# Performance work log

Hardware: AMD Instinct MI355X
Metric: run time of the kernel (lower is better)

## Reference

```python
import jax, jax.numpy as jnp
import numpy as np

BETA = 1.0 / np.sqrt(768.0).astype(np.float32)


def setup_inputs() -> dict:
    key = jax.random.key(0)
    k1, k2, k3 = jax.random.split(key, 3)
    x = jax.random.normal(k1, (32, 512, 768), dtype=jnp.float32)
    # torch nn.Linear(dim, n_prototype).weight has shape [n_prototype, dim]
    w_lookup = jax.random.normal(k2, (4096, 768), dtype=jnp.float32) * 0.02
    # torch nn.Linear(n_prototype, dim).weight has shape [dim, n_prototype]
    w_content = jax.random.normal(k3, (768, 4096), dtype=jnp.float32) * 0.02
    return {"x": x, "w_lookup": w_lookup, "w_content": w_content}


def reference(x, w_lookup, w_content):
    # scores: [b, s, n_prototype] = x @ w_lookup^T, scaled by 1/sqrt(dim)
    scores = jnp.einsum("bsd,pd->bsp", x, w_lookup) * jnp.asarray(BETA, x.dtype)
    lookup = jax.nn.softmax(scores, axis=-1)
    # content: [b, s, dim] = lookup @ w_content^T
    content = jnp.einsum("bsp,dp->bsd", lookup, w_content)
    return content  # dropout is identity in eval / p=0.0
```

## Files before the change

kernel.cpp:

```cpp
#include <hip/hip_runtime.h>
#include <hip/hip_bf16.h>


#define NTOK   16384
#define DIM    768
#define NPROT  4096
#define BETA_F 0.03608439182428583f

typedef __bf16 bf16_t;
typedef __bf16 bf16x8 __attribute__((ext_vector_type(8)));
typedef float  floatx4 __attribute__((ext_vector_type(4)));

__device__ __forceinline__ void async_copy16(const bf16_t* g, void* l) {
  __builtin_amdgcn_global_load_lds(
      (__attribute__((address_space(1))) const void*)g,
      (__attribute__((address_space(3))) void*)l, 16, 0, 0);
}

__global__ __launch_bounds__(256) void cvt_all(
    const float* __restrict__ x, const float* __restrict__ wl,
    const float* __restrict__ wc, bf16_t* __restrict__ xb,
    bf16_t* __restrict__ wlb, bf16_t* __restrict__ wcb,
    int nx8, int nw8, int nc8) {
  int i = blockIdx.x * 256 + threadIdx.x;
  const float* in; bf16_t* out; int k; int dv;
  if (i < nx8) {
    in = x; out = xb; k = i;
    const int m = k / 96, kv = k % 96;
    const int kt = kv >> 3, kr = kv & 7;
    const int sf = (((m >> 4) & 15) << 1) + (kr >> 2);
    const int l  = (m & 15) + ((kr & 3) << 4);
    dv = (((m >> 8) * 12 + kt) * 32 + sf) * 64 + l;
  } else if (i < nx8 + nw8) {
    in = wl; out = wlb; k = i - nx8;
    const int p = k / 96, kv = k % 96;
    const int kt = kv >> 3, kr = kv & 7;
    const int sf = (((p >> 4) & 15) << 1) + (kr >> 2);
    const int l  = (p & 15) + ((kr & 3) << 4);
    dv = (((p >> 8) * 12 + kt) * 32 + sf) * 64 + l;
  } else if (i < nx8 + nw8 + nc8) {
    in = wc; out = wcb; k = i - nx8 - nw8;
    const int d = k / 512, pv = k % 512;
    const int kt = pv >> 3, kr = pv & 7;
    const int dd = d % 192;
    const int sf = ((dd >> 4) << 1) + (kr >> 2);
    const int l  = (dd & 15) + ((kr & 3) << 4);
    dv = (((d / 192) * 64 + kt) * 24 + sf) * 64 + l;
  } else return;
  const float4* in4 = (const float4*)in;
  float4 a = in4[2 * k], b = in4[2 * k + 1];
  bf16x8 o;
  o[0] = (bf16_t)a.x; o[1] = (bf16_t)a.y; o[2] = (bf16_t)a.z; o[3] = (bf16_t)a.w;
  o[4] = (bf16_t)b.x; o[5] = (bf16_t)b.y; o[6] = (bf16_t)b.z; o[7] = (bf16_t)b.w;
  ((bf16x8*)out)[dv] = o;
}

__global__ __launch_bounds__(512, 2)
void gemm256(const bf16_t* __restrict__ A, const bf16_t* __restrict__ B,
             bf16_t* __restrict__ P, float* __restrict__ rowsum,
             const int K, const int N, const int nN) {
  __shared__ char lds[131072];

  const int tid = threadIdx.x;
  const int l   = tid & 63;
  const int w   = tid >> 6;
  const int wr  = w >> 2;
  const int wc  = w & 3;
  const int lr  = l & 15;

  const int nwg   = gridDim.x;
  const int chunk = nwg >> 3;
  const int wg    = (blockIdx.x & 7) * chunk + (blockIdx.x >> 3);
  const int m0    = (wg / nN) * 256;
  const int n0    = (wg % nN) * 256;

  const int T = K >> 6;
  const int abase = (m0 >> 8) * T * 16384 + l * 8;
  const int bbase = (n0 >> 8) * T * 16384 + l * 8;
  int asf[2][2];
#pragma unroll
  for (int h = 0; h < 2; ++h)
#pragma unroll
    for (int j = 0; j < 2; ++j) {
      const int s = j * 8 + w;
      asf[h][j] = ((h * 8 + (s >> 1)) * 2 + (s & 1)) * 512;
    }

  auto stageA = [&](int slot, int kt, int h) {
#pragma unroll
    for (int j = 0; j < 2; ++j) {
      const int s  = j * 8 + w;
      const int sf = (h * 8 + (s >> 1)) * 2 + (s & 1);
      async_copy16(A + abase + kt * 16384 + asf[h][j],
                   lds + slot * 65536 + sf * 1024);
    }
  };
  auto stageB = [&](int slot, int kt, int h) {
#pragma unroll
    for (int j = 0; j < 2; ++j) {
      const int s  = j * 8 + w;
      const int sf = (h * 8 + (s >> 1)) * 2 + (s & 1);
      async_copy16(B + bbase + kt * 16384 + asf[h][j],
                   lds + slot * 65536 + 32768 + sf * 1024);
    }
  };

  bf16x8 af[4][2], bg[4][2];
  auto loadA = [&](int slot, int mh) {
#pragma unroll
    for (int q = 0; q < 4; ++q)
#pragma unroll
      for (int ks = 0; ks < 2; ++ks)
        af[q][ks] = *(const bf16x8*)(lds + slot * 65536 +
                        ((mh * 8 + q * 2 + wr) * 2 + ks) * 1024 + l * 16);
  };
  auto loadB = [&](int slot, int nh, int qb) {
#pragma unroll
    for (int q = 0; q < 2; ++q)
#pragma unroll
      for (int ks = 0; ks < 2; ++ks)
        bg[qb + q][ks] = *(const bf16x8*)(lds + slot * 65536 + 32768 +
                        ((nh * 8 + q * 4 + wc) * 2 + ks) * 1024 + l * 16);
  };

  const floatx4 z = {0.f, 0.f, 0.f, 0.f};
  floatx4 acc[8][4];
#pragma unroll
  for (int mt = 0; mt < 8; ++mt)
#pragma unroll
    for (int nt = 0; nt < 4; ++nt) acc[mt][nt] = z;

  auto mma = [&](int mq, int nq) {
    __builtin_amdgcn_s_setprio(1);
#pragma unroll
    for (int q = 0; q < 4; ++q)
#pragma unroll
      for (int r = 0; r < 2; ++r)
#pragma unroll
        for (int ks = 0; ks < 2; ++ks)
          acc[mq * 4 + q][nq * 2 + r] = __builtin_amdgcn_mfma_f32_16x16x32_bf16(
              af[q][ks], bg[nq * 2 + r][ks], acc[mq * 4 + q][nq * 2 + r], 0, 0, 0);
    __builtin_amdgcn_s_setprio(0);
  };

#define BAR()    __builtin_amdgcn_s_barrier()
#define LGKM0()  asm volatile("s_waitcnt lgkmcnt(0)")
#define LGKM8()  asm volatile("s_waitcnt lgkmcnt(8)")
#define VM(n)    asm volatile("s_waitcnt vmcnt(" #n ")" ::: "memory")

  stageA(0, 0, 0); stageB(0, 0, 0); stageB(0, 0, 1); stageA(0, 0, 1);
  stageA(1, 1, 0); stageB(1, 1, 0); stageB(1, 1, 1);
  VM(6);
  BAR();

#pragma unroll 1
  for (int t = 0; t < T - 2; t += 2) {
    loadA(0, 0); loadB(0, 0, 0);
    stageA(1, t + 1, 1);
    LGKM8();
    BAR(); LGKM0(); mma(0, 0); BAR();
    loadB(0, 1, 2);
    stageA(0, t + 2, 0);
    BAR(); LGKM0(); mma(0, 1); BAR();
    loadA(0, 1);
    stageB(0, t + 2, 0);
    BAR(); LGKM0(); mma(1, 1); BAR();
    stageB(0, t + 2, 1);
    BAR(); mma(1, 0); VM(6); BAR();
    loadA(1, 0); loadB(1, 0, 0);
    stageA(0, t + 2, 1);
    LGKM8();
    BAR(); LGKM0(); mma(0, 0); BAR();
    loadB(1, 1, 2);
    stageA(1, t + 3, 0);
    BAR(); LGKM0(); mma(0, 1); BAR();
    loadA(1, 1);
    stageB(1, t + 3, 0);
    BAR(); LGKM0(); mma(1, 1); BAR();
    stageB(1, t + 3, 1);
    BAR(); mma(1, 0); VM(6); BAR();
  }

  loadA(0, 0); loadB(0, 0, 0);
  stageA(1, T - 1, 1);
  LGKM8();
  BAR(); LGKM0(); mma(0, 0); BAR();
  loadB(0, 1, 2);
  BAR(); LGKM0(); mma(0, 1); BAR();
  loadA(0, 1);
  BAR(); LGKM0(); mma(1, 1); BAR();
  BAR(); mma(1, 0); VM(0); BAR();
  loadA(1, 0); loadB(1, 0, 0);
  BAR(); LGKM0(); mma(0, 0); BAR();
  loadB(1, 1, 2);
  BAR(); LGKM0(); mma(0, 1); BAR();
  loadA(1, 1);
  BAR(); LGKM0(); mma(1, 1); BAR();
  mma(1, 0);

#undef BAR
#undef LGKM0
#undef LGKM8
#undef VM

  __syncthreads();
  bf16_t* pl = (bf16_t*)lds;
  const int hi4 = (l >> 4) << 2;
#pragma unroll
  for (int mt = 0; mt < 8; ++mt) {
    const int rl = (mt * 2 + wr) * 16 + hi4;
    float rs[4] = {0.f, 0.f, 0.f, 0.f};
#pragma unroll
    for (int nt = 0; nt < 4; ++nt) {
      const int cl = (nt * 4 + wc) * 16 + lr;
#pragma unroll
      for (int i = 0; i < 4; ++i) {
        const float e = __expf(acc[mt][nt][i] * BETA_F);
        pl[(rl + i) * 256 + cl] = (bf16_t)e;
        rs[i] += e;
      }
    }
#pragma unroll
    for (int i = 0; i < 4; ++i) {
      float s = rs[i];
      s += __shfl_xor(s, 1);
      s += __shfl_xor(s, 2);
      s += __shfl_xor(s, 4);
      s += __shfl_xor(s, 8);
      if (lr == 0) atomicAdd(&rowsum[m0 + rl + i], s);
    }
  }
  __syncthreads();
#pragma unroll
  for (int it = 0; it < 16; ++it) {
    const int idx = it * 512 + tid;
    const int rr  = idx >> 5;
    const int cc  = (idx & 31) << 3;
    bf16x8 v = *(const bf16x8*)(pl + rr * 256 + cc);
    *(bf16x8*)(P + (size_t)(m0 + rr) * N + n0 + cc) = v;
  }
}

__global__ __launch_bounds__(512, 2)
void gemm192(const bf16_t* __restrict__ A, const bf16_t* __restrict__ B,
             float* __restrict__ O, const float* __restrict__ rowsum,
             const int K, const int N) {
  __shared__ char lds[114688];

  const int tid = threadIdx.x;
  const int l   = tid & 63;
  const int w   = tid >> 6;
  const int wr  = w >> 2;
  const int wc  = w & 3;
  const int lr  = l & 15;
  const int lk  = (l >> 4) << 3;

  const int wg = (blockIdx.x & 7) * 32 + (blockIdx.x >> 3);
  const int m0 = (wg >> 2) * 256;
  const int n0 = (wg & 3) * 192;

  int aoff[2][2];
#pragma unroll
  for (int h = 0; h < 2; ++h)
#pragma unroll
    for (int j = 0; j < 2; ++j) {
      const int s     = j * 8 + w;
      const int mfrag = h * 8 + (s >> 1);
      const int ks    = s & 1;
      aoff[h][j] = (m0 + mfrag * 16 + lr) * K + ks * 32 + lk;
    }
  const int bb = (n0 / 192) * 64 * 12288 + l * 8;
  int bsf[3];
#pragma unroll
  for (int t = 0; t < 3; ++t) bsf[t] = (t * 8 + w) * 512;

  auto stageA = [&](int slot, int kt, int h) {
#pragma unroll
    for (int j = 0; j < 2; ++j) {
      const int s  = j * 8 + w;
      const int sf = (h * 8 + (s >> 1)) * 2 + (s & 1);
      async_copy16(A + aoff[h][j] + kt * 64, lds + slot * 57344 + sf * 1024);
    }
  };
  auto stageBt = [&](int slot, int kt, int t) {
    async_copy16(B + bb + kt * 12288 + bsf[t],
                 lds + slot * 57344 + 32768 + (t * 8 + w) * 1024 + l * 16);
  };

  bf16x8 af[4][2], bg[3][2];
  auto loadA = [&](int slot, int mh) {
#pragma unroll
    for (int q = 0; q < 4; ++q)
#pragma unroll
      for (int ks = 0; ks < 2; ++ks)
        af[q][ks] = *(const bf16x8*)(lds + slot * 57344 +
                        ((mh * 8 + q * 2 + wr) * 2 + ks) * 1024 + l * 16);
  };
  auto loadBn = [&](int slot, int nlo, int ncnt) {
    for (int r = 0; r < ncnt; ++r)
#pragma unroll
      for (int ks = 0; ks < 2; ++ks)
        bg[nlo + r][ks] = *(const bf16x8*)(lds + slot * 57344 + 32768 +
                        (((wc * 3 + nlo + r) * 2 + ks) << 10) + l * 16);
  };

  const floatx4 z = {0.f, 0.f, 0.f, 0.f};
  floatx4 acc[8][3];
#pragma unroll
  for (int mt = 0; mt < 8; ++mt)
#pragma unroll
    for (int nt = 0; nt < 3; ++nt) acc[mt][nt] = z;

  auto mma = [&](int mq, int nlo, int ncnt) {
    __builtin_amdgcn_s_setprio(1);
#pragma unroll
    for (int q = 0; q < 4; ++q)
      for (int r = 0; r < ncnt; ++r)
#pragma unroll
        for (int ks = 0; ks < 2; ++ks)
          acc[mq * 4 + q][nlo + r] = __builtin_amdgcn_mfma_f32_16x16x32_bf16(
              af[q][ks], bg[nlo + r][ks], acc[mq * 4 + q][nlo + r], 0, 0, 0);
    __builtin_amdgcn_s_setprio(0);
  };

#define BAR()    __builtin_amdgcn_s_barrier()
#define LGKM0()  asm volatile("s_waitcnt lgkmcnt(0)")
#define LGKM8()  asm volatile("s_waitcnt lgkmcnt(8)")
#define VM(n)    asm volatile("s_waitcnt vmcnt(" #n ")" ::: "memory")

  const int T = K >> 6;

  stageA(0, 0, 0); stageA(0, 0, 1);
  stageBt(0, 0, 0); stageBt(0, 0, 1); stageBt(0, 0, 2);
  stageA(1, 1, 0);
  stageBt(1, 1, 0); stageBt(1, 1, 1); stageBt(1, 1, 2);
  VM(5);
  BAR();

#pragma unroll 1
  for (int t = 0; t < T - 2; t += 2) {
#pragma unroll
    for (int u = 0; u < 2; ++u) {
      const int p = u;
      loadA(p, 0); loadBn(p, 0, 2);
      stageA(p ^ 1, t + u + 1, 1);
      LGKM8();
      BAR(); LGKM0(); mma(0, 0, 2); BAR();
      loadBn(p, 2, 1);
      stageA(p, t + u + 2, 0);
      BAR(); LGKM0(); mma(0, 2, 1); BAR();
      loadA(p, 1);
      stageBt(p, t + u + 2, 0); stageBt(p, t + u + 2, 1);
      BAR(); LGKM0(); mma(1, 0, 2); BAR();
      stageBt(p, t + u + 2, 2);
      BAR(); mma(1, 2, 1); VM(5); BAR();
    }
  }

  loadA(0, 0); loadBn(0, 0, 2);
  stageA(1, T - 1, 1);
  LGKM8();
  BAR(); LGKM0(); mma(0, 0, 2); BAR();
  loadBn(0, 2, 1);
  BAR(); LGKM0(); mma(0, 2, 1); BAR();
  loadA(0, 1);
  BAR(); LGKM0(); mma(1, 0, 2); BAR();
  BAR(); mma(1, 2, 1); VM(0); BAR();
  loadA(1, 0); loadBn(1, 0, 2);
  BAR(); LGKM0(); mma(0, 0, 2); BAR();
  loadBn(1, 2, 1);
  BAR(); LGKM0(); mma(0, 2, 1); BAR();
  loadA(1, 1);
  BAR(); LGKM0(); mma(1, 0, 2); BAR();
  mma(1, 2, 1);

#undef BAR
#undef LGKM0
#undef LGKM8
#undef VM

  const int hi4 = (l >> 4) << 2;
#pragma unroll
  for (int mt = 0; mt < 8; ++mt) {
    const int row = m0 + (mt * 2 + wr) * 16 + hi4;
#pragma unroll
    for (int i = 0; i < 4; ++i) {
      const float inv = 1.0f / rowsum[row + i];
#pragma unroll
      for (int nt = 0; nt < 3; ++nt)
        O[(row + i) * N + n0 + (wc * 3 + nt) * 16 + lr] = acc[mt][nt][i] * inv;
    }
  }
}

__global__ __launch_bounds__(256) void hopfield_fallback(
    const float* __restrict__ x, const float* __restrict__ wl,
    const float* __restrict__ wc, float* __restrict__ out) {
  __shared__ float  xs[8 * 768];
  __shared__ bf16_t ps[8 * 4096];
  __shared__ float  rs[8];
  const int tid = threadIdx.x;
  const int r0  = blockIdx.x * 8;
  if (tid < 8) rs[tid] = 0.f;
  for (int i = tid; i < 8 * 768; i += 256)
    xs[i] = x[(r0 + (i / 768)) * 768 + (i % 768)];
  __syncthreads();

  float lsum[8] = {0, 0, 0, 0, 0, 0, 0, 0};
  for (int p = tid; p < 4096; p += 256) {
    float s[8] = {0, 0, 0, 0, 0, 0, 0, 0};
    for (int d = 0; d < 768; ++d) {
      const float wv = wl[p * 768 + d];
#pragma unroll
      for (int r = 0; r < 8; ++r) s[r] += xs[r * 768 + d] * wv;
    }
#pragma unroll
    for (int r = 0; r < 8; ++r) {
      const float e = __expf(s[r] * BETA_F);
      ps[r * 4096 + p] = (bf16_t)e;
      lsum[r] += e;
    }
  }
#pragma unroll
  for (int r = 0; r < 8; ++r) atomicAdd(&rs[r], lsum[r]);
  __syncthreads();

  for (int d = tid; d < 768; d += 256) {
    float o[8] = {0, 0, 0, 0, 0, 0, 0, 0};
    for (int p = 0; p < 4096; ++p) {
      const float wv = wc[d * 4096 + p];
#pragma unroll
      for (int r = 0; r < 8; ++r) o[r] += (float)ps[r * 4096 + p] * wv;
    }
#pragma unroll
    for (int r = 0; r < 8; ++r) out[(r0 + r) * 768 + d] = o[r] / rs[r];
  }
}

extern "C" void kernel_launch(void* const* d_in, const int* in_sizes, int n_in,
                              void* d_out, int out_size, void* d_ws, size_t ws_size,
                              hipStream_t stream) {
  (void)in_sizes; (void)n_in; (void)out_size;
  const float* x  = (const float*)d_in[0];
  const float* wl = (const float*)d_in[1];
  const float* wc = (const float*)d_in[2];
  float* out = (float*)d_out;

  const size_t xb_e = (size_t)NTOK * DIM;
  const size_t wl_e = (size_t)NPROT * DIM;
  const size_t wc_e = (size_t)DIM * NPROT;
  const size_t P_e  = (size_t)NTOK * NPROT;
  const size_t need = (xb_e + wl_e + wc_e + P_e) * 2 + (size_t)NTOK * 4;

  if (ws_size >= need) {
    char* ws = (char*)d_ws;
    bf16_t* xb  = (bf16_t*)ws;  ws += xb_e * 2;
    bf16_t* wlb = (bf16_t*)ws;  ws += wl_e * 2;
    bf16_t* wcb = (bf16_t*)ws;  ws += wc_e * 2;
    bf16_t* P   = (bf16_t*)ws;  ws += P_e * 2;
    float* rowsum = (float*)ws;

    hipMemsetAsync(rowsum, 0, NTOK * sizeof(float), stream);
    const int nx8 = (int)(xb_e / 8), nw8 = (int)(wl_e / 8), nc8 = (int)(wc_e / 8);
    cvt_all<<<(nx8 + nw8 + nc8 + 255) / 256, 256, 0, stream>>>(
        x, wl, wc, xb, wlb, wcb, nx8, nw8, nc8);
    gemm256<<<dim3((NTOK / 256) * (NPROT / 256)), 512, 0, stream>>>(
        xb, wlb, P, rowsum, DIM, NPROT, NPROT / 256);
    gemm192<<<dim3(256), 512, 0, stream>>>(
        P, wcb, out, rowsum, NPROT, DIM);
  } else {
    hopfield_fallback<<<NTOK / 8, 256, 0, stream>>>(x, wl, wc, out);
  }
}
```

Before: 388.2 us.

## Restructure GEMM main loops into two-phase schedule with full B fragment loads

```diff
diff --git a/kernel.cpp b/kernel.cpp
--- a/kernel.cpp
+++ b/kernel.cpp
@@ -114,13 +114,15 @@
         af[q][ks] = *(const bf16x8*)(lds + slot * 65536 +
                         ((mh * 8 + q * 2 + wr) * 2 + ks) * 1024 + l * 16);
   };
-  auto loadB = [&](int slot, int nh, int qb) {
-#pragma unroll
-    for (int q = 0; q < 2; ++q)
-#pragma unroll
-      for (int ks = 0; ks < 2; ++ks)
-        bg[qb + q][ks] = *(const bf16x8*)(lds + slot * 65536 + 32768 +
-                        ((nh * 8 + q * 4 + wc) * 2 + ks) * 1024 + l * 16);
+  auto loadB = [&](int slot) {
+#pragma unroll
+    for (int nh = 0; nh < 2; ++nh)
+#pragma unroll
+      for (int q = 0; q < 2; ++q)
+#pragma unroll
+        for (int ks = 0; ks < 2; ++ks)
+          bg[nh * 2 + q][ks] = *(const bf16x8*)(lds + slot * 65536 + 32768 +
+                          ((nh * 8 + q * 4 + wc) * 2 + ks) * 1024 + l * 16);
   };
 
   const floatx4 z = {0.f, 0.f, 0.f, 0.f};
@@ -130,77 +132,57 @@
 #pragma unroll
     for (int nt = 0; nt < 4; ++nt) acc[mt][nt] = z;
 
-  auto mma = [&](int mq, int nq) {
+  auto mma2 = [&](int mq) {
     __builtin_amdgcn_s_setprio(1);
 #pragma unroll
-    for (int q = 0; q < 4; ++q)
-#pragma unroll
-      for (int r = 0; r < 2; ++r)
-#pragma unroll
-        for (int ks = 0; ks < 2; ++ks)
-          acc[mq * 4 + q][nq * 2 + r] = __builtin_amdgcn_mfma_f32_16x16x32_bf16(
-              af[q][ks], bg[nq * 2 + r][ks], acc[mq * 4 + q][nq * 2 + r], 0, 0, 0);
+    for (int ks = 0; ks < 2; ++ks)
+#pragma unroll
+      for (int q = 0; q < 4; ++q)
+#pragma unroll
+        for (int nt = 0; nt < 4; ++nt)
+          acc[mq * 4 + q][nt] = __builtin_amdgcn_mfma_f32_16x16x32_bf16(
+              af[q][ks], bg[nt][ks], acc[mq * 4 + q][nt], 0, 0, 0);
     __builtin_amdgcn_s_setprio(0);
   };
 
 #define BAR()    __builtin_amdgcn_s_barrier()
 #define LGKM0()  asm volatile("s_waitcnt lgkmcnt(0)")
-#define LGKM8()  asm volatile("s_waitcnt lgkmcnt(8)")
 #define VM(n)    asm volatile("s_waitcnt vmcnt(" #n ")" ::: "memory")
 
-  stageA(0, 0, 0); stageB(0, 0, 0); stageB(0, 0, 1); stageA(0, 0, 1);
+  stageA(0, 0, 0); stageA(0, 0, 1); stageB(0, 0, 0); stageB(0, 0, 1);
   stageA(1, 1, 0); stageB(1, 1, 0); stageB(1, 1, 1);
   VM(6);
   BAR();
 
 #pragma unroll 1
-  for (int t = 0; t < T - 2; t += 2) {
-    loadA(0, 0); loadB(0, 0, 0);
-    stageA(1, t + 1, 1);
-    LGKM8();
-    BAR(); LGKM0(); mma(0, 0); BAR();
-    loadB(0, 1, 2);
-    stageA(0, t + 2, 0);
-    BAR(); LGKM0(); mma(0, 1); BAR();
-    loadA(0, 1);
-    stageB(0, t + 2, 0);
-    BAR(); LGKM0(); mma(1, 1); BAR();
-    stageB(0, t + 2, 1);
-    BAR(); mma(1, 0); VM(6); BAR();
-    loadA(1, 0); loadB(1, 0, 0);
-    stageA(0, t + 2, 1);
-    LGKM8();
-    BAR(); LGKM0(); mma(0, 0); BAR();
-    loadB(1, 1, 2);
-    stageA(1, t + 3, 0);
-    BAR(); LGKM0(); mma(0, 1); BAR();
-    loadA(1, 1);
-    stageB(1, t + 3, 0);
-    BAR(); LGKM0(); mma(1, 1); BAR();
-    stageB(1, t + 3, 1);
-    BAR(); mma(1, 0); VM(6); BAR();
-  }
-
-  loadA(0, 0); loadB(0, 0, 0);
-  stageA(1, T - 1, 1);
-  LGKM8();
-  BAR(); LGKM0(); mma(0, 0); BAR();
-  loadB(0, 1, 2);
-  BAR(); LGKM0(); mma(0, 1); BAR();
-  loadA(0, 1);
-  BAR(); LGKM0(); mma(1, 1); BAR();
-  BAR(); mma(1, 0); VM(0); BAR();
-  loadA(1, 0); loadB(1, 0, 0);
-  BAR(); LGKM0(); mma(0, 0); BAR();
-  loadB(1, 1, 2);
-  BAR(); LGKM0(); mma(0, 1); BAR();
-  loadA(1, 1);
-  BAR(); LGKM0(); mma(1, 1); BAR();
-  mma(1, 0);
+  for (int t = 0; t < T - 2; ++t) {
+    const int p = t & 1;
+    loadA(p, 0); loadB(p);
+    stageA(p ^ 1, t + 1, 1);
+    BAR(); LGKM0(); mma2(0); BAR();
+    loadA(p, 1);
+    stageA(p, t + 2, 0);
+    stageB(p, t + 2, 0); stageB(p, t + 2, 1);
+    BAR(); LGKM0(); mma2(1);
+    VM(6);
+    BAR();
+  }
+
+  {
+    const int p = (T - 2) & 1;
+    loadA(p, 0); loadB(p);
+    stageA(p ^ 1, T - 1, 1);
+    BAR(); LGKM0(); mma2(0); BAR();
+    loadA(p, 1);
+    BAR(); LGKM0(); mma2(1); VM(0); BAR();
+    loadA(p ^ 1, 0); loadB(p ^ 1);
+    BAR(); LGKM0(); mma2(0); BAR();
+    loadA(p ^ 1, 1);
+    BAR(); LGKM0(); mma2(1);
+  }
 
 #undef BAR
 #undef LGKM0
-#undef LGKM8
 #undef VM
 
   __syncthreads();
@@ -296,12 +278,13 @@
         af[q][ks] = *(const bf16x8*)(lds + slot * 57344 +
                         ((mh * 8 + q * 2 + wr) * 2 + ks) * 1024 + l * 16);
   };
-  auto loadBn = [&](int slot, int nlo, int ncnt) {
-    for (int r = 0; r < ncnt; ++r)
+  auto loadBall = [&](int slot) {
+#pragma unroll
+    for (int r = 0; r < 3; ++r)
 #pragma unroll
       for (int ks = 0; ks < 2; ++ks)
-        bg[nlo + r][ks] = *(const bf16x8*)(lds + slot * 57344 + 32768 +
-                        (((wc * 3 + nlo + r) * 2 + ks) << 10) + l * 16);
+        bg[r][ks] = *(const bf16x8*)(lds + slot * 57344 + 32768 +
+                        (((wc * 3 + r) * 2 + ks) << 10) + l * 16);
   };
 
   const floatx4 z = {0.f, 0.f, 0.f, 0.f};
@@ -311,21 +294,21 @@
 #pragma unroll
     for (int nt = 0; nt < 3; ++nt) acc[mt][nt] = z;
 
-  auto mma = [&](int mq, int nlo, int ncnt) {
+  auto mma2 = [&](int mq) {
     __builtin_amdgcn_s_setprio(1);
 #pragma unroll
-    for (int q = 0; q < 4; ++q)
-      for (int r = 0; r < ncnt; ++r)
-#pragma unroll
-        for (int ks = 0; ks < 2; ++ks)
-          acc[mq * 4 + q][nlo + r] = __builtin_amdgcn_mfma_f32_16x16x32_bf16(
-              af[q][ks], bg[nlo + r][ks], acc[mq * 4 + q][nlo + r], 0, 0, 0);
+    for (int ks = 0; ks < 2; ++ks)
+#pragma unroll
+      for (int q = 0; q < 4; ++q)
+#pragma unroll
+        for (int nt = 0; nt < 3; ++nt)
+          acc[mq * 4 + q][nt] = __builtin_amdgcn_mfma_f32_16x16x32_bf16(
+              af[q][ks], bg[nt][ks], acc[mq * 4 + q][nt], 0, 0, 0);
     __builtin_amdgcn_s_setprio(0);
   };
 
 #define BAR()    __builtin_amdgcn_s_barrier()
 #define LGKM0()  asm volatile("s_waitcnt lgkmcnt(0)")
-#define LGKM8()  asm volatile("s_waitcnt lgkmcnt(8)")
 #define VM(n)    asm volatile("s_waitcnt vmcnt(" #n ")" ::: "memory")
 
   const int T = K >> 6;
@@ -338,45 +321,34 @@
   BAR();
 
 #pragma unroll 1
-  for (int t = 0; t < T - 2; t += 2) {
-#pragma unroll
-    for (int u = 0; u < 2; ++u) {
-      const int p = u;
-      loadA(p, 0); loadBn(p, 0, 2);
-      stageA(p ^ 1, t + u + 1, 1);
-      LGKM8();
-      BAR(); LGKM0(); mma(0, 0, 2); BAR();
-      loadBn(p, 2, 1);
-      stageA(p, t + u + 2, 0);
-      BAR(); LGKM0(); mma(0, 2, 1); BAR();
-      loadA(p, 1);
-      stageBt(p, t + u + 2, 0); stageBt(p, t + u + 2, 1);
-      BAR(); LGKM0(); mma(1, 0, 2); BAR();
-      stageBt(p, t + u + 2, 2);
-      BAR(); mma(1, 2, 1); VM(5); BAR();
-    }
-  }
-
-  loadA(0, 0); loadBn(0, 0, 2);
-  stageA(1, T - 1, 1);
-  LGKM8();
-  BAR(); LGKM0(); mma(0, 0, 2); BAR();
-  loadBn(0, 2, 1);
-  BAR(); LGKM0(); mma(0, 2, 1); BAR();
-  loadA(0, 1);
-  BAR(); LGKM0(); mma(1, 0, 2); BAR();
-  BAR(); mma(1, 2, 1); VM(0); BAR();
-  loadA(1, 0); loadBn(1, 0, 2);
-  BAR(); LGKM0(); mma(0, 0, 2); BAR();
-  loadBn(1, 2, 1);
-  BAR(); LGKM0(); mma(0, 2, 1); BAR();
-  loadA(1, 1);
-  BAR(); LGKM0(); mma(1, 0, 2); BAR();
-  mma(1, 2, 1);
+  for (int t = 0; t < T - 2; ++t) {
+    const int p = t & 1;
+    loadA(p, 0); loadBall(p);
+    stageA(p ^ 1, t + 1, 1);
+    BAR(); LGKM0(); mma2(0); BAR();
+    loadA(p, 1);
+    stageA(p, t + 2, 0);
+    stageBt(p, t + 2, 0); stageBt(p, t + 2, 1); stageBt(p, t + 2, 2);
+    BAR(); LGKM0(); mma2(1);
+    VM(5);
+    BAR();
+  }
+
+  {
+    const int p = (T - 2) & 1;
+    loadA(p, 0); loadBall(p);
+    stageA(p ^ 1, T - 1, 1);
+    BAR(); LGKM0(); mma2(0); BAR();
+    loadA(p, 1);
+    BAR(); LGKM0(); mma2(1); VM(0); BAR();
+    loadA(p ^ 1, 0); loadBall(p ^ 1);
+    BAR(); LGKM0(); mma2(0); BAR();
+    loadA(p ^ 1, 1);
+    BAR(); LGKM0(); mma2(1);
+  }
 
 #undef BAR
 #undef LGKM0
-#undef LGKM8
 #undef VM
 
   const int hi4 = (l >> 4) << 2;
```

Measured after the change: 400.4 us. 1.03x slower.
